# Optimization experiments

Measured on AMD Instinct MI355X. Metric: run time of the kernel, lower is better.

## Reference

```python
import jax, jax.numpy as jnp
import numpy as np

D_MODEL = 2048
NUM_HEADS = 16
HEAD_DIM = D_MODEL // NUM_HEADS  # 128
ROPE_BASE = 10000.0
B, L = 2, 2048


def _rope_tables(seq_len, head_dim, base):
    # inv_freq over even dims; cos/sin tables of shape (seq_len, head_dim)
    inv_freq = 1.0 / (base ** (jnp.arange(0, head_dim, 2, dtype=jnp.float32) / head_dim))
    t = jnp.arange(seq_len, dtype=jnp.float32)
    freqs = jnp.einsum('l,d->ld', t, inv_freq)          # (L, head_dim/2)
    emb = jnp.concatenate([freqs, freqs], axis=-1)       # (L, head_dim)
    return jnp.cos(emb), jnp.sin(emb)


def _apply_rope(x, cos, sin):
    # x: (B, H, L, d); rotate-half convention
    d = x.shape[-1]
    x1, x2 = x[..., : d // 2], x[..., d // 2:]
    rotated = jnp.concatenate([-x2, x1], axis=-1)
    return x * cos + rotated * sin


def setup_inputs() -> dict:
    key = jax.random.key(0)
    k0, k1, k2 = jax.random.split(key, 3)
    query = jax.random.normal(k0, (B, L, D_MODEL), dtype=jnp.float32)
    W_qkv = jax.random.normal(k1, (3 * D_MODEL, D_MODEL), dtype=jnp.float32) * 0.02
    b_qkv = jnp.zeros((3 * D_MODEL,), dtype=jnp.float32)
    W_out = jax.random.normal(k2, (D_MODEL, D_MODEL), dtype=jnp.float32) * 0.02
    b_out = jnp.zeros((D_MODEL,), dtype=jnp.float32)
    return {"query": query, "W_qkv": W_qkv, "b_qkv": b_qkv, "W_out": W_out, "b_out": b_out}


def reference(query, W_qkv, b_qkv, W_out, b_out):
    Bq, Lq, _ = query.shape
    # fused QKV projection (single matmul)
    qkv = jnp.einsum('bld,ed->ble', query, W_qkv) + b_qkv  # (B, L, 3D)
    q, k, v = jnp.split(qkv, 3, axis=-1)

    def shape_heads(x):
        return x.reshape(Bq, Lq, NUM_HEADS, HEAD_DIM).transpose(0, 2, 1, 3)  # (B,H,L,d)

    q, k, v = shape_heads(q), shape_heads(k), shape_heads(v)

    cos, sin = _rope_tables(Lq, HEAD_DIM, ROPE_BASE)
    q = _apply_rope(q, cos, sin)
    k = _apply_rope(k, cos, sin)

    scale = 1.0 / jnp.sqrt(jnp.asarray(HEAD_DIM, dtype=q.dtype))
    scores = jnp.einsum('bhqd,bhkd->bhqk', q, k) * scale  # (B,H,L,L)
    causal = jnp.tril(jnp.ones((Lq, Lq), dtype=bool))
    scores = jnp.where(causal, scores, jnp.finfo(scores.dtype).min)
    probs = jax.nn.softmax(scores, axis=-1)
    attn = jnp.einsum('bhqk,bhkd->bhqd', probs, v)        # (B,H,L,d)

    out = attn.transpose(0, 2, 1, 3).reshape(Bq, Lq, D_MODEL)
    return jnp.einsum('bld,ed->ble', out, W_out) + b_out
```

## Files before the change

### kernel.cpp

```cpp
#include <hip/hip_runtime.h>

typedef unsigned short u16;
typedef unsigned int u32;
typedef __bf16 bf16x8 __attribute__((ext_vector_type(8)));
typedef float f32x4 __attribute__((ext_vector_type(4)));

__device__ __forceinline__ u16 f2b(float f) {
  u32 u = __float_as_uint(f);
  u32 r = (u + 0x7fffu + ((u >> 16) & 1u)) >> 16;
  return (u16)r;
}
__device__ __forceinline__ float b2f(u16 v) {
  return __uint_as_float(((u32)v) << 16);
}

__global__ __launch_bounds__(256) void convert_all(
    const float4* __restrict__ q, const float4* __restrict__ w1,
    const float4* __restrict__ w2, ushort4* __restrict__ out) {
  int i = blockIdx.x * 256 + threadIdx.x;
  float4 f;
  if (i < 2097152) f = q[i];
  else if (i < 5242880) f = w1[i - 2097152];
  else f = w2[i - 5242880];
  ushort4 o;
  o.x = f2b(f.x); o.y = f2b(f.y); o.z = f2b(f.z); o.w = f2b(f.w);
  out[i] = o;
}

template <int OUT_BF16>
__global__ __launch_bounds__(256) void gemm_bt(
    const u16* __restrict__ A, const u16* __restrict__ B,
    const float* __restrict__ bias, void* __restrict__ Cv,
    int M, int N, int K) {
  __shared__ __align__(16) u16 As[128 * 64];
  __shared__ __align__(16) u16 Bs[128 * 64];
  const int tid = threadIdx.x;
  const int lane = tid & 63;
  const int wave = tid >> 6;
  const int m0 = blockIdx.y * 128;
  const int n0 = blockIdx.x * 128;
  const int wm = (wave & 1) * 64;
  const int wn = (wave >> 1) * 64;
  f32x4 acc[4][4] = {};

  const int srow = wave * 32 + (lane >> 3);
  const int scb = ((lane & 7) ^ (lane >> 3)) * 16;
  const int fr = lane & 15;
  const int g = lane >> 4;

  const int kiters = K >> 6;
  for (int kt = 0; kt < kiters; ++kt) {
    const int k0 = kt << 6;
    __syncthreads();
    {
      const char* gA = (const char*)A + ((size_t)(m0 + srow) * K + k0) * 2 + scb;
      const char* gB = (const char*)B + ((size_t)(n0 + srow) * K + k0) * 2 + scb;
#pragma unroll
      for (int i = 0; i < 4; ++i) {
        __builtin_amdgcn_global_load_lds(
            (__attribute__((address_space(1))) void*)(gA + (size_t)i * 8 * K * 2),
            (__attribute__((address_space(3))) void*)(As + (wave * 32 + i * 8) * 64),
            16, 0, 0);
        __builtin_amdgcn_global_load_lds(
            (__attribute__((address_space(1))) void*)(gB + (size_t)i * 8 * K * 2),
            (__attribute__((address_space(3))) void*)(Bs + (wave * 32 + i * 8) * 64),
            16, 0, 0);
      }
    }
    __syncthreads();
#pragma unroll
    for (int ks = 0; ks < 2; ++ks) {
      const int so = ((ks * 4 + g) ^ (fr & 7)) * 8;
      bf16x8 aF[4], bF[4];
#pragma unroll
      for (int mi = 0; mi < 4; ++mi)
        __builtin_memcpy(&aF[mi], &As[(wm + mi * 16 + fr) * 64 + so], 16);
#pragma unroll
      for (int ni = 0; ni < 4; ++ni)
        __builtin_memcpy(&bF[ni], &Bs[(wn + ni * 16 + fr) * 64 + so], 16);
#pragma unroll
      for (int mi = 0; mi < 4; ++mi)
#pragma unroll
        for (int ni = 0; ni < 4; ++ni)
          acc[mi][ni] = __builtin_amdgcn_mfma_f32_16x16x32_bf16(aF[mi], bF[ni], acc[mi][ni], 0, 0, 0);
    }
  }
  const int rq = (lane >> 4) * 4;
  const int cq = lane & 15;
#pragma unroll
  for (int mi = 0; mi < 4; ++mi) {
#pragma unroll
    for (int ni = 0; ni < 4; ++ni) {
      int col = n0 + wn + ni * 16 + cq;
      float bs = bias[col];
#pragma unroll
      for (int i = 0; i < 4; ++i) {
        int row = m0 + wm + mi * 16 + rq + i;
        float v = acc[mi][ni][i] + bs;
        if (OUT_BF16)
          ((u16*)Cv)[(size_t)row * N + col] = f2b(v);
        else
          ((float*)Cv)[(size_t)row * N + col] = v;
      }
    }
  }
}

__global__ __launch_bounds__(256) void rope_reshape(
    const u16* __restrict__ qkv, u16* __restrict__ qh, u16* __restrict__ kh) {
  int idx = blockIdx.x * 256 + threadIdx.x;
  int i = idx & 63;
  int h = (idx >> 6) & 15;
  int l = (idx >> 10) & 2047;
  int b = idx >> 21;
  const u16* row = qkv + ((size_t)(b * 2048 + l)) * 6144;
  int off = h * 128 + i;
  float q1 = b2f(row[off]), q2 = b2f(row[off + 64]);
  float k1 = b2f(row[2048 + off]), k2 = b2f(row[2048 + off + 64]);
  float inv = exp2f(-(float)i * 0.20762050593046869f);
  float ang = (float)l * inv;
  float s, c;
  sincosf(ang, &s, &c);
  size_t o = ((size_t)(b * 16 + h) * 2048 + l) * 128;
  const float qs = 0.08838834764831845f;
  qh[o + i]      = f2b((q1 * c - q2 * s) * qs);
  qh[o + 64 + i] = f2b((q2 * c + q1 * s) * qs);
  kh[o + i]      = f2b(k1 * c - k2 * s);
  kh[o + 64 + i] = f2b(k2 * c + k1 * s);
}

__global__ __launch_bounds__(256) void transpose_v(
    const u16* __restrict__ qkv, u16* __restrict__ vhT) {
  __shared__ u16 Ts[64 * 65];
  const int tid = threadIdx.x;
  const int lt = blockIdx.x;
  const int dh = blockIdx.y;
  const int bh = blockIdx.z;
  const int b = bh >> 4, h = bh & 15;
  const int l0 = lt * 64, d0 = dh * 64;
#pragma unroll
  for (int it = 0; it < 16; ++it) {
    int idx = it * 256 + tid;
    int l = idx >> 6, d = idx & 63;
    Ts[l * 65 + d] =
        qkv[((size_t)(b * 2048 + l0 + l)) * 6144 + 4096 + h * 128 + d0 + d];
  }
  __syncthreads();
#pragma unroll
  for (int it = 0; it < 16; ++it) {
    int idx = it * 256 + tid;
    int d = idx >> 6, l = idx & 63;
    vhT[((size_t)bh * 128 + d0 + d) * 2048 + l0 + l] = Ts[l * 65 + d];
  }
}

__global__ __launch_bounds__(256, 2) void attn_flash(
    const u16* __restrict__ qh, const u16* __restrict__ kh,
    const u16* __restrict__ vhT, u16* __restrict__ oh) {
  __shared__ __align__(16) u16 Ks[64 * 128];
  __shared__ __align__(16) u16 Vt[128 * 64];
  __shared__ __align__(16) u16 Ps[128 * 72];
  const int tid = threadIdx.x;
  const int lane = tid & 63;
  const int w = tid >> 6;
  const int cq = lane & 15;
  const int g = lane >> 4;
  const int p = blockIdx.x;
  const int bh = blockIdx.y;
  const int b = bh >> 4, h = bh & 15;
  const int ktiles = 32 - p;
  int q0s[2];
  q0s[0] = p * 64;
  q0s[1] = (31 - p) * 64;

  bf16x8 qf[2][4];
#pragma unroll
  for (int s = 0; s < 2; ++s) {
    const u16* qp = qh + ((size_t)bh * 2048 + q0s[s] + w * 16 + cq) * 128 + g * 8;
#pragma unroll
    for (int ks = 0; ks < 4; ++ks)
      __builtin_memcpy(&qf[s][ks], qp + ks * 32, 16);
  }

  f32x4 o[2][8] = {};
  float mrow[2] = {-1e30f, -1e30f};
  float lrow[2] = {0.0f, 0.0f};

  const int krl = lane >> 4;
  const int kcl = lane & 15;
  const int vrl = lane >> 3;
  const int vcl = lane & 7;

  for (int kt = 0; kt < ktiles; ++kt) {
    __syncthreads();
    {
      const size_t kvb = (size_t)bh * 2048 + (size_t)kt * 64;
#pragma unroll
      for (int i = 0; i < 4; ++i) {
        int row = w * 16 + i * 4 + krl;
        int cgl = kcl ^ (row & 7);
        const char* src = (const char*)(kh + (kvb + row) * 128 + cgl * 8);
        __builtin_amdgcn_global_load_lds(
            (__attribute__((address_space(1))) void*)src,
            (__attribute__((address_space(3))) void*)(Ks + (w * 16 + i * 4) * 128),
            16, 0, 0);
      }
#pragma unroll
      for (int i = 0; i < 4; ++i) {
        int row = w * 32 + i * 8 + vrl;
        int cgl = vcl ^ (row & 7);
        const char* src =
            (const char*)(vhT + ((size_t)bh * 128 + row) * 2048 + kt * 64 + cgl * 8);
        __builtin_amdgcn_global_load_lds(
            (__attribute__((address_space(1))) void*)src,
            (__attribute__((address_space(3))) void*)(Vt + (w * 32 + i * 8) * 64),
            16, 0, 0);
      }
    }
    __syncthreads();

    const bool nA = (kt <= p);
    f32x4 S[4][2] = {};
#pragma unroll
    for (int ks = 0; ks < 4; ++ks) {
#pragma unroll
      for (int mt = 0; mt < 4; ++mt) {
        bf16x8 kf;
        int slot = (ks * 4 + g) ^ (cq & 7);
        __builtin_memcpy(&kf, &Ks[(mt * 16 + cq) * 128 + slot * 8], 16);
        if (nA)
          S[mt][0] = __builtin_amdgcn_mfma_f32_16x16x32_bf16(kf, qf[0][ks], S[mt][0], 0, 0, 0);
        S[mt][1] = __builtin_amdgcn_mfma_f32_16x16x32_bf16(kf, qf[1][ks], S[mt][1], 0, 0, 0);
      }
    }

#pragma unroll
    for (int s = 0; s < 2; ++s) {
      if (s == 0 && !nA) continue;
      const int dtile = s ? (ktiles - 1) : p;
      if (kt == dtile) {
        const int qg = q0s[s] + w * 16 + cq;
#pragma unroll
        for (int mt = 0; mt < 4; ++mt)
#pragma unroll
          for (int i = 0; i < 4; ++i)
            if (kt * 64 + mt * 16 + g * 4 + i > qg) S[mt][s][i] = -1e30f;
      }
      float mx = S[0][s][0];
#pragma unroll
      for (int mt = 0; mt < 4; ++mt)
#pragma unroll
        for (int i = 0; i < 4; ++i) mx = fmaxf(mx, S[mt][s][i]);
      mx = fmaxf(mx, __shfl_xor(mx, 16));
      mx = fmaxf(mx, __shfl_xor(mx, 32));
      float mnew = fmaxf(mrow[s], mx);
      float al = __expf(mrow[s] - mnew);
      mrow[s] = mnew;
      float rs = 0.0f;
#pragma unroll
      for (int mt = 0; mt < 4; ++mt) {
        float e0 = __expf(S[mt][s][0] - mnew);
        float e1 = __expf(S[mt][s][1] - mnew);
        float e2 = __expf(S[mt][s][2] - mnew);
        float e3 = __expf(S[mt][s][3] - mnew);
        rs += (e0 + e1) + (e2 + e3);
        ushort4 pk;
        pk.x = f2b(e0); pk.y = f2b(e1); pk.z = f2b(e2); pk.w = f2b(e3);
        *(ushort4*)&Ps[(s * 64 + w * 16 + cq) * 72 + mt * 16 + g * 4] = pk;
      }
      rs += __shfl_xor(rs, 16);
      rs += __shfl_xor(rs, 32);
      lrow[s] = lrow[s] * al + rs;
#pragma unroll
      for (int dmt = 0; dmt < 8; ++dmt) {
        o[s][dmt][0] *= al; o[s][dmt][1] *= al;
        o[s][dmt][2] *= al; o[s][dmt][3] *= al;
      }
    }

#pragma unroll
    for (int ks = 0; ks < 2; ++ks) {
      bf16x8 pf0, pf1;
      if (nA) __builtin_memcpy(&pf0, &Ps[(w * 16 + cq) * 72 + ks * 32 + g * 8], 16);
      __builtin_memcpy(&pf1, &Ps[(64 + w * 16 + cq) * 72 + ks * 32 + g * 8], 16);
#pragma unroll
      for (int dmt = 0; dmt < 8; ++dmt) {
        bf16x8 vf;
        int slot = (ks * 4 + g) ^ (cq & 7);
        __builtin_memcpy(&vf, &Vt[(dmt * 16 + cq) * 64 + slot * 8], 16);
        if (nA)
          o[0][dmt] = __builtin_amdgcn_mfma_f32_16x16x32_bf16(vf, pf0, o[0][dmt], 0, 0, 0);
        o[1][dmt] = __builtin_amdgcn_mfma_f32_16x16x32_bf16(vf, pf1, o[1][dmt], 0, 0, 0);
      }
    }
  }

#pragma unroll
  for (int s = 0; s < 2; ++s) {
    float inv = 1.0f / lrow[s];
    int qg = q0s[s] + w * 16 + cq;
    size_t base = ((size_t)(b * 2048 + qg)) * 2048 + h * 128;
#pragma unroll
    for (int dmt = 0; dmt < 8; ++dmt) {
      ushort4 t;
      t.x = f2b(o[s][dmt][0] * inv);
      t.y = f2b(o[s][dmt][1] * inv);
      t.z = f2b(o[s][dmt][2] * inv);
      t.w = f2b(o[s][dmt][3] * inv);
      *(ushort4*)(oh + base + dmt * 16 + g * 4) = t;
    }
  }
}

extern "C" void kernel_launch(void* const* d_in, const int* in_sizes, int n_in,
                              void* d_out, int out_size, void* d_ws, size_t ws_size,
                              hipStream_t stream) {
  (void)in_sizes; (void)n_in; (void)out_size; (void)ws_size;
  const float* query = (const float*)d_in[0];
  const float* W_qkv = (const float*)d_in[1];
  const float* b_qkv = (const float*)d_in[2];
  const float* W_out = (const float*)d_in[3];
  const float* b_out = (const float*)d_in[4];
  float* out = (float*)d_out;
  char* ws = (char*)d_ws;

  u16* Abf  = (u16*)(ws + 0);
  u16* W1bf = (u16*)(ws + (size_t)16777216);
  u16* W2bf = (u16*)(ws + (size_t)41943040);
  u16* QKV  = (u16*)(ws + (size_t)50331648);
  u16* qhp  = (u16*)(ws + (size_t)100663296);
  u16* khp  = (u16*)(ws + (size_t)117440512);
  u16* vhT  = (u16*)(ws + (size_t)134217728);
  u16* ohp  = (u16*)(ws + (size_t)150994944);

  convert_all<<<24576, 256, 0, stream>>>((const float4*)query, (const float4*)W_qkv,
                                         (const float4*)W_out, (ushort4*)ws);
  gemm_bt<1><<<dim3(48, 32), 256, 0, stream>>>(Abf, W1bf, b_qkv, (void*)QKV, 4096, 6144, 2048);
  rope_reshape<<<16384, 256, 0, stream>>>(QKV, qhp, khp);
  transpose_v<<<dim3(32, 2, 32), 256, 0, stream>>>(QKV, vhT);
  attn_flash<<<dim3(16, 32), 256, 0, stream>>>(qhp, khp, vhT, ohp);
  gemm_bt<0><<<dim3(16, 32), 256, 0, stream>>>(ohp, W2bf, b_out, (void*)out, 4096, 2048, 2048);
}
```

Baseline: 386.2 us.

## Fuse RoPE, head reshape and V transpose into QKV GEMM epilogue

The QKV projection GEMM now stages its output tile in shared memory and writes rotated/scaled Q and K in head layout, and transposed V, directly. The separate rope_reshape and transpose_v kernels and the intermediate QKV buffer are removed. RoPE cos/sin come from a small precomputed table kernel instead of per-element sincos. This avoids a full round trip of the 48 MB bf16 QKV tensor through memory plus two launches, at the cost of a heavier GEMM epilogue with scattered narrow stores.

```diff
diff --git a/kernel.cpp b/kernel.cpp
--- a/kernel.cpp
+++ b/kernel.cpp
@@ -27,10 +27,129 @@
   out[i] = o;
 }
 
-template <int OUT_BF16>
+__global__ __launch_bounds__(256) void rope_tab(float2* __restrict__ tab) {
+  int idx = blockIdx.x * 256 + threadIdx.x;
+  int l = idx >> 6, dp = idx & 63;
+  float inv = exp2f(-(float)dp * 0.20762050593046869f);
+  float ang = (float)l * inv;
+  float s, c;
+  sincosf(ang, &s, &c);
+  tab[idx] = make_float2(c, s);
+}
+
+__global__ __launch_bounds__(256) void gemm_qkv(
+    const u16* __restrict__ A, const u16* __restrict__ B,
+    const float* __restrict__ bias, const float2* __restrict__ tab,
+    u16* __restrict__ qh, u16* __restrict__ kh, u16* __restrict__ vhT) {
+  __shared__ __align__(16) u16 sh[16512];
+  u16* As = sh;
+  u16* Bs = sh + 8192;
+  const int K = 2048;
+  const int tid = threadIdx.x;
+  const int lane = tid & 63;
+  const int wave = tid >> 6;
+  const int m0 = blockIdx.y * 128;
+  const int n0 = blockIdx.x * 128;
+  const int wm = (wave & 1) * 64;
+  const int wn = (wave >> 1) * 64;
+  f32x4 acc[4][4] = {};
+
+  const int srow = wave * 32 + (lane >> 3);
+  const int scb = ((lane & 7) ^ (lane >> 3)) * 16;
+  const int fr = lane & 15;
+  const int g = lane >> 4;
+
+  for (int kt = 0; kt < 32; ++kt) {
+    const int k0 = kt << 6;
+    __syncthreads();
+    {
+      const char* gA = (const char*)A + ((size_t)(m0 + srow) * K + k0) * 2 + scb;
+      const char* gB = (const char*)B + ((size_t)(n0 + srow) * K + k0) * 2 + scb;
+#pragma unroll
+      for (int i = 0; i < 4; ++i) {
+        __builtin_amdgcn_global_load_lds(
+            (__attribute__((address_space(1))) void*)(gA + (size_t)i * 8 * K * 2),
+            (__attribute__((address_space(3))) void*)(As + (wave * 32 + i * 8) * 64),
+            16, 0, 0);
+        __builtin_amdgcn_global_load_lds(
+            (__attribute__((address_space(1))) void*)(gB + (size_t)i * 8 * K * 2),
+            (__attribute__((address_space(3))) void*)(Bs + (wave * 32 + i * 8) * 64),
+            16, 0, 0);
+      }
+    }
+    __syncthreads();
+#pragma unroll
+    for (int ks = 0; ks < 2; ++ks) {
+      const int so = ((ks * 4 + g) ^ (fr & 7)) * 8;
+      bf16x8 aF[4], bF[4];
+#pragma unroll
+      for (int mi = 0; mi < 4; ++mi)
+        __builtin_memcpy(&aF[mi], &As[(wm + mi * 16 + fr) * 64 + so], 16);
+#pragma unroll
+      for (int ni = 0; ni < 4; ++ni)
+        __builtin_memcpy(&bF[ni], &Bs[(wn + ni * 16 + fr) * 64 + so], 16);
+#pragma unroll
+      for (int mi = 0; mi < 4; ++mi)
+#pragma unroll
+        for (int ni = 0; ni < 4; ++ni)
+          acc[mi][ni] = __builtin_amdgcn_mfma_f32_16x16x32_bf16(aF[mi], bF[ni], acc[mi][ni], 0, 0, 0);
+    }
+  }
+
+  __syncthreads();
+  const int rq = (lane >> 4) * 4;
+  const int cq = lane & 15;
+#pragma unroll
+  for (int mi = 0; mi < 4; ++mi) {
+#pragma unroll
+    for (int ni = 0; ni < 4; ++ni) {
+      int c = wn + ni * 16 + cq;
+      float bs = bias[n0 + c];
+#pragma unroll
+      for (int i = 0; i < 4; ++i) {
+        int r = wm + mi * 16 + rq + i;
+        sh[r * 129 + c] = f2b(acc[mi][ni][i] + bs);
+      }
+    }
+  }
+  __syncthreads();
+
+  const int t = n0 >> 7;
+  const int h = t & 15;
+  const int bq = m0 >> 11;
+  const int l0 = m0 & 2047;
+  const int bh = bq * 16 + h;
+
+  if (t < 32) {
+    const float qs = (t < 16) ? 0.08838834764831845f : 1.0f;
+    u16* dst = (t < 16) ? qh : kh;
+#pragma unroll 4
+    for (int it = 0; it < 32; ++it) {
+      int idx = it * 256 + tid;
+      int l = idx >> 6, dp = idx & 63;
+      float2 cs = tab[(size_t)(l0 + l) * 64 + dp];
+      float x1 = b2f(sh[l * 129 + dp]);
+      float x2 = b2f(sh[l * 129 + dp + 64]);
+      size_t o = ((size_t)bh * 2048 + l0 + l) * 128;
+      dst[o + dp]      = f2b((x1 * cs.x - x2 * cs.y) * qs);
+      dst[o + dp + 64] = f2b((x2 * cs.x + x1 * cs.y) * qs);
+    }
+  } else {
+#pragma unroll 4
+    for (int it = 0; it < 32; ++it) {
+      int idx = it * 256 + tid;
+      int d = idx >> 6, l2 = (idx & 63) * 2;
+      ushort2 t2;
+      t2.x = sh[l2 * 129 + d];
+      t2.y = sh[(l2 + 1) * 129 + d];
+      *(ushort2*)(vhT + ((size_t)bh * 128 + d) * 2048 + l0 + l2) = t2;
+    }
+  }
+}
+
 __global__ __launch_bounds__(256) void gemm_bt(
     const u16* __restrict__ A, const u16* __restrict__ B,
-    const float* __restrict__ bias, void* __restrict__ Cv,
+    const float* __restrict__ bias, float* __restrict__ C,
     int M, int N, int K) {
   __shared__ __align__(16) u16 As[128 * 64];
   __shared__ __align__(16) u16 Bs[128 * 64];
@@ -96,61 +215,9 @@
 #pragma unroll
       for (int i = 0; i < 4; ++i) {
         int row = m0 + wm + mi * 16 + rq + i;
-        float v = acc[mi][ni][i] + bs;
-        if (OUT_BF16)
-          ((u16*)Cv)[(size_t)row * N + col] = f2b(v);
-        else
-          ((float*)Cv)[(size_t)row * N + col] = v;
-      }
-    }
-  }
-}
-
-__global__ __launch_bounds__(256) void rope_reshape(
-    const u16* __restrict__ qkv, u16* __restrict__ qh, u16* __restrict__ kh) {
-  int idx = blockIdx.x * 256 + threadIdx.x;
-  int i = idx & 63;
-  int h = (idx >> 6) & 15;
-  int l = (idx >> 10) & 2047;
-  int b = idx >> 21;
-  const u16* row = qkv + ((size_t)(b * 2048 + l)) * 6144;
-  int off = h * 128 + i;
-  float q1 = b2f(row[off]), q2 = b2f(row[off + 64]);
-  float k1 = b2f(row[2048 + off]), k2 = b2f(row[2048 + off + 64]);
-  float inv = exp2f(-(float)i * 0.20762050593046869f);
-  float ang = (float)l * inv;
-  float s, c;
-  sincosf(ang, &s, &c);
-  size_t o = ((size_t)(b * 16 + h) * 2048 + l) * 128;
-  const float qs = 0.08838834764831845f;
-  qh[o + i]      = f2b((q1 * c - q2 * s) * qs);
-  qh[o + 64 + i] = f2b((q2 * c + q1 * s) * qs);
-  kh[o + i]      = f2b(k1 * c - k2 * s);
-  kh[o + 64 + i] = f2b(k2 * c + k1 * s);
-}
-
-__global__ __launch_bounds__(256) void transpose_v(
-    const u16* __restrict__ qkv, u16* __restrict__ vhT) {
-  __shared__ u16 Ts[64 * 65];
-  const int tid = threadIdx.x;
-  const int lt = blockIdx.x;
-  const int dh = blockIdx.y;
-  const int bh = blockIdx.z;
-  const int b = bh >> 4, h = bh & 15;
-  const int l0 = lt * 64, d0 = dh * 64;
-#pragma unroll
-  for (int it = 0; it < 16; ++it) {
-    int idx = it * 256 + tid;
-    int l = idx >> 6, d = idx & 63;
-    Ts[l * 65 + d] =
-        qkv[((size_t)(b * 2048 + l0 + l)) * 6144 + 4096 + h * 128 + d0 + d];
-  }
-  __syncthreads();
-#pragma unroll
-  for (int it = 0; it < 16; ++it) {
-    int idx = it * 256 + tid;
-    int d = idx >> 6, l = idx & 63;
-    vhT[((size_t)bh * 128 + d0 + d) * 2048 + l0 + l] = Ts[l * 65 + d];
+        C[(size_t)row * N + col] = acc[mi][ni][i] + bs;
+      }
+    }
   }
 }
 
@@ -324,20 +391,19 @@
   float* out = (float*)d_out;
   char* ws = (char*)d_ws;
 
-  u16* Abf  = (u16*)(ws + 0);
-  u16* W1bf = (u16*)(ws + (size_t)16777216);
-  u16* W2bf = (u16*)(ws + (size_t)41943040);
-  u16* QKV  = (u16*)(ws + (size_t)50331648);
-  u16* qhp  = (u16*)(ws + (size_t)100663296);
-  u16* khp  = (u16*)(ws + (size_t)117440512);
-  u16* vhT  = (u16*)(ws + (size_t)134217728);
-  u16* ohp  = (u16*)(ws + (size_t)150994944);
+  u16*    Abf  = (u16*)(ws + 0);
+  u16*    W1bf = (u16*)(ws + (size_t)16777216);
+  u16*    W2bf = (u16*)(ws + (size_t)41943040);
+  u16*    qhp  = (u16*)(ws + (size_t)50331648);
+  u16*    khp  = (u16*)(ws + (size_t)67108864);
+  u16*    vhT  = (u16*)(ws + (size_t)83886080);
+  u16*    ohp  = (u16*)(ws + (size_t)100663296);
+  float2* tab  = (float2*)(ws + (size_t)117440512);
 
   convert_all<<<24576, 256, 0, stream>>>((const float4*)query, (const float4*)W_qkv,
                                          (const float4*)W_out, (ushort4*)ws);
-  gemm_bt<1><<<dim3(48, 32), 256, 0, stream>>>(Abf, W1bf, b_qkv, (void*)QKV, 4096, 6144, 2048);
-  rope_reshape<<<16384, 256, 0, stream>>>(QKV, qhp, khp);
-  transpose_v<<<dim3(32, 2, 32), 256, 0, stream>>>(QKV, vhT);
+  rope_tab<<<512, 256, 0, stream>>>(tab);
+  gemm_qkv<<<dim3(48, 32), 256, 0, stream>>>(Abf, W1bf, b_qkv, tab, qhp, khp, vhT);
   attn_flash<<<dim3(16, 32), 256, 0, stream>>>(qhp, khp, vhT, ohp);
-  gemm_bt<0><<<dim3(16, 32), 256, 0, stream>>>(ohp, W2bf, b_out, (void*)out, 4096, 2048, 2048);
-}
+  gemm_bt<<<dim3(16, 32), 256, 0, stream>>>(ohp, W2bf, b_out, out, 4096, 2048, 2048);
+}
```

Measured after the change: 380.5 us. No clear change (-1.5%).
